# Kernel tuning notes

Measured on AMD Instinct MI355X. Metric: run time of the kernel, lower is better.

Reference implementation:

```python
import jax, jax.numpy as jnp
import numpy as np

BATCH, SEQ, D_IN, D_OUT = 32, 1024, 128, 128
NEG_SLOPE = 0.1


def setup_inputs() -> dict:
    key = jax.random.key(0)
    k1, k2, k3, k4 = jax.random.split(key, 4)
    nodes = jax.random.normal(k1, (BATCH, SEQ, D_IN), dtype=jnp.float32)
    adjacent = jax.random.randint(k2, (BATCH, SEQ, SEQ), 0, 2, dtype=jnp.int32)
    W = jax.random.normal(k3, (D_IN, D_OUT), dtype=jnp.float32) / np.sqrt(D_IN)
    B = jax.random.normal(k4, (D_IN, D_OUT), dtype=jnp.float32) / np.sqrt(D_IN)
    return {"nodes": nodes, "adjacent": adjacent, "W": W, "B": B}


def reference(nodes, adjacent, W, B):
    # mask[b, out, in] = 1 if edge (out -> in) present
    mask = (adjacent != 0).astype(nodes.dtype)
    # counts[b, in] = in-degree (number of 'out' neighbors pooled per target node)
    counts = mask.sum(axis=1)                               # [b, s_in]
    # segment-sum of neighbor features: pooled[b, in, d] = sum_out mask * nodes[b, out, d]
    pooled = jnp.einsum('boi,bod->bid', mask, nodes)        # [b, s_in, d]
    # mean over neighbors; nodes with zero degree get no pooled contribution
    pooled = jnp.where(counts[..., None] > 0,
                       pooled / jnp.maximum(counts, 1.0)[..., None],
                       jnp.zeros((), dtype=nodes.dtype))
    updated = nodes @ B + pooled @ W                        # [b, s, d_out]
    return jax.nn.leaky_relu(updated, negative_slope=NEG_SLOPE)
```

## Files before the change

### kernel.cpp

```cpp
#include <hip/hip_runtime.h>
#include <hip/hip_bf16.h>

#define SEQ 1024
#define DIM 128
#define NEG_SLOPE 0.1f

typedef __bf16 bf16x8 __attribute__((ext_vector_type(8)));
typedef float f32x4v __attribute__((ext_vector_type(4)));
typedef unsigned char uchar;

#define MASKQ_BYTES ((size_t)32 * 1024 * 1024)
#define NTQ_BYTES   ((size_t)32 * 128 * 1024)

__device__ __forceinline__ unsigned short bfb(float f) {
    __bf16 h = (__bf16)f;
    return __builtin_bit_cast(unsigned short, h);
}


__device__ __forceinline__ uchar f32_to_e4m3(float f) {
#if __has_builtin(__builtin_amdgcn_cvt_pk_fp8_f32)
    int r = __builtin_amdgcn_cvt_pk_fp8_f32(f, f, 0, false);
    return (uchar)(r & 0xff);
#else
    unsigned u = __builtin_bit_cast(unsigned, f);
    unsigned s = (u >> 24) & 0x80;
    int e = (u >> 23) & 0xff;
    unsigned m = u & 0x7fffff;
    int te = e - 120;
    if (te >= 1) {
        unsigned keep = m >> 20, rest = m & 0xfffff;
        keep += (rest > 0x80000u) || (rest == 0x80000u && (keep & 1));
        if (keep == 8) { keep = 0; ++te; }
        if (te > 15) return (uchar)(s | 0x7e);
        return (uchar)(s | (te << 3) | keep);
    }
    float af = f < 0 ? -f : f;
    int q = (int)(af * 512.0f + 0.5f);
    if (q > 7) q = 7;
    return (uchar)(s | q);
#endif
}

__global__ __launch_bounds__(256)
void transpose_adj(const int* __restrict__ adj, uchar* __restrict__ mq)
{
    __shared__ uchar lds[64][72];
    const int b  = blockIdx.x >> 8;
    const int ot = (blockIdx.x >> 4) & 15;
    const int it = blockIdx.x & 15;
    const int o0 = ot << 6, i0 = it << 6;
    const int t  = threadIdx.x;

    const int r0 = (t >> 4) << 2;
    const int c0 = (t & 15) << 2;
    const int* pa = adj + ((size_t)(b * SEQ + o0 + r0)) * SEQ + i0 + c0;
    int4 A[4];
    #pragma unroll
    for (int r = 0; r < 4; ++r) A[r] = *(const int4*)(pa + (size_t)r * SEQ);

    #pragma unroll
    for (int c = 0; c < 4; ++c) {
        unsigned w = 0;
        w |= (((const int*)&A[0])[c] != 0 ? 0x38u : 0u);
        w |= (((const int*)&A[1])[c] != 0 ? 0x38u : 0u) << 8;
        w |= (((const int*)&A[2])[c] != 0 ? 0x38u : 0u) << 16;
        w |= (((const int*)&A[3])[c] != 0 ? 0x38u : 0u) << 24;
        *(unsigned*)&lds[c0 + c][r0] = w;
    }
    __syncthreads();

    const int i_loc = t >> 2;
    const int quad  = t & 3;
    const uint2 lo = *(const uint2*)&lds[i_loc][quad * 8];
    const uint2 hi = *(const uint2*)&lds[i_loc][32 + quad * 8];
    uint4 outv; outv.x = lo.x; outv.y = lo.y; outv.z = hi.x; outv.w = hi.y;
    *(uint4*)(mq + ((size_t)(b * SEQ + i0 + i_loc)) * SEQ + o0 + quad * 16) = outv;
}

__global__ __launch_bounds__(256)
void transpose_nodes(const float* __restrict__ nodes, uchar* __restrict__ nq)
{
    __shared__ float lds[64][33];
    const int b  = blockIdx.x >> 6;
    const int ot = (blockIdx.x >> 2) & 15;
    const int dt = blockIdx.x & 3;
    const int o0 = ot << 6, d0 = dt << 5;
    const int t  = threadIdx.x;

    const float* src = nodes + ((size_t)(b * SEQ + o0)) * DIM + d0;
    #pragma unroll
    for (int p = 0; p < 8; ++p) {
        const int o = (t >> 5) + p * 8;
        const int d = t & 31;
        lds[o][d] = src[(size_t)o * DIM + d];
    }
    __syncthreads();

    const int d_loc = t >> 3;
    const int p0    = (t & 7) * 8;
    const int quad  = (t & 7) >> 1;
    const int half  = t & 1;
    const int ob    = half * 32 + quad * 8;
    union { uchar b[8]; uint2 u; } pk;
    #pragma unroll
    for (int j = 0; j < 8; ++j) pk.b[j] = f32_to_e4m3(lds[ob + j][d_loc]);
    *(uint2*)(nq + ((size_t)(b * DIM + d0 + d_loc)) * SEQ + o0 + p0) = pk.u;
}

__global__ __launch_bounds__(256)
void transpose_wb(const float* __restrict__ W, const float* __restrict__ Bm,
                  unsigned short* __restrict__ wt, unsigned short* __restrict__ bt)
{
    const int which = blockIdx.x & 1;
    const int slice = blockIdx.x >> 1;
    const float* in = which ? Bm : W;
    unsigned short* out = which ? bt : wt;
    const int base = slice * 1024;
    #pragma unroll
    for (int r = 0; r < 4; ++r) {
        const int idx = base + r * 256 + threadIdx.x;
        const int d = idx >> 7, k = idx & 127;
        out[idx] = bfb(in[k * DIM + d]);
    }
}

__device__ __forceinline__ long mk64(unsigned lo, unsigned hi) {
    return (long)(((unsigned long long)hi << 32) | lo);
}

__global__ __launch_bounds__(256, 2)
void gcn_main(const float* __restrict__ nodes,
              const uchar* __restrict__ mq,
              const uchar* __restrict__ nq,
              const unsigned short* __restrict__ wt,
              const unsigned short* __restrict__ bt,
              float* __restrict__ out)
{
    __shared__ unsigned short pooled[64][136];

    const int bid   = blockIdx.x;
    const int xcd   = bid & 7;
    const int slot  = bid >> 3;
    const int batch = ((slot >> 4) << 3) | xcd;
    const int mtile = slot & 15;
    const int i0    = mtile << 6;

    const int tid  = threadIdx.x;
    const int wave = tid >> 6;
    const int lane = tid & 63;
    const int wm   = wave >> 1;
    const int wn   = wave & 1;
    const int lrow = lane & 15;
    const int quad = lane >> 4;

    const uchar* __restrict__ mq_b = mq + (size_t)batch * SEQ * SEQ;
    const uchar* __restrict__ nq_b = nq + (size_t)batch * DIM * SEQ;
    const float* __restrict__ nodes_b = nodes + (size_t)batch * SEQ * DIM;

    f32x4v acc[2][4] = {};
    f32x4v acc_cnt[2] = {};
    const long ones = 0x3838383838383838L;

    const uchar* pa0 = mq_b + (size_t)(i0 + wm * 32 + lrow) * SEQ + quad * 16;
    const uchar* pb0 = nq_b + (size_t)(wn * 64 + lrow) * SEQ + quad * 16;

    #pragma unroll 4
    for (int n = 0; n < 16; ++n) {
        const int off = n * 64;
        uint4 a4[2], b4[4];
        #pragma unroll
        for (int mf = 0; mf < 2; ++mf)
            a4[mf] = *(const uint4*)(pa0 + (size_t)mf * 16 * SEQ + off);
        #pragma unroll
        for (int nf = 0; nf < 4; ++nf)
            b4[nf] = *(const uint4*)(pb0 + (size_t)nf * 16 * SEQ + off);
        #pragma unroll
        for (int half = 0; half < 2; ++half) {
            long a64[2], b64[4];
            #pragma unroll
            for (int mf = 0; mf < 2; ++mf)
                a64[mf] = half ? mk64(a4[mf].z, a4[mf].w) : mk64(a4[mf].x, a4[mf].y);
            #pragma unroll
            for (int nf = 0; nf < 4; ++nf)
                b64[nf] = half ? mk64(b4[nf].z, b4[nf].w) : mk64(b4[nf].x, b4[nf].y);
            #pragma unroll
            for (int mf = 0; mf < 2; ++mf) {
                #pragma unroll
                for (int nf = 0; nf < 4; ++nf)
                    acc[mf][nf] = __builtin_amdgcn_mfma_f32_16x16x32_fp8_fp8(
                        a64[mf], b64[nf], acc[mf][nf], 0, 0, 0);
                acc_cnt[mf] = __builtin_amdgcn_mfma_f32_16x16x32_fp8_fp8(
                    a64[mf], ones, acc_cnt[mf], 0, 0, 0);
            }
        }
    }

    #pragma unroll
    for (int mf = 0; mf < 2; ++mf) {
        #pragma unroll
        for (int r = 0; r < 4; ++r) {
            const int row = wm * 32 + mf * 16 + quad * 4 + r;
            const float cnt = acc_cnt[mf][r];
            const float inv = (cnt > 0.5f) ? 1.0f / cnt : 0.0f;
            #pragma unroll
            for (int nf = 0; nf < 4; ++nf) {
                const int col = wn * 64 + nf * 16 + lrow;
                pooled[row][col] = bfb(acc[mf][nf][r] * inv);
            }
        }
    }
    __syncthreads();

    f32x4v acc2[2][4] = {};
    const int d_b0 = wn * 64 + lrow;

    #pragma unroll
    for (int ks = 0; ks < 4; ++ks) {
        const int k0 = ks * 32 + quad * 8;
        bf16x8 av[2], av2[2], bw[4], bb[4];
        #pragma unroll
        for (int mf = 0; mf < 2; ++mf) {
            av[mf] = *(const bf16x8*)&pooled[wm * 32 + mf * 16 + lrow][k0];
            const float* p = nodes_b + (size_t)(i0 + wm * 32 + mf * 16 + lrow) * DIM + k0;
            const float4 f1 = *(const float4*)p;
            const float4 f2 = *(const float4*)(p + 4);
            av2[mf][0] = (__bf16)f1.x; av2[mf][1] = (__bf16)f1.y;
            av2[mf][2] = (__bf16)f1.z; av2[mf][3] = (__bf16)f1.w;
            av2[mf][4] = (__bf16)f2.x; av2[mf][5] = (__bf16)f2.y;
            av2[mf][6] = (__bf16)f2.z; av2[mf][7] = (__bf16)f2.w;
        }
        #pragma unroll
        for (int nf = 0; nf < 4; ++nf) {
            bw[nf] = *(const bf16x8*)(wt + (size_t)(d_b0 + nf * 16) * DIM + k0);
            bb[nf] = *(const bf16x8*)(bt + (size_t)(d_b0 + nf * 16) * DIM + k0);
        }
        #pragma unroll
        for (int mf = 0; mf < 2; ++mf)
            #pragma unroll
            for (int nf = 0; nf < 4; ++nf) {
                acc2[mf][nf] = __builtin_amdgcn_mfma_f32_16x16x32_bf16(av[mf],  bw[nf], acc2[mf][nf], 0, 0, 0);
                acc2[mf][nf] = __builtin_amdgcn_mfma_f32_16x16x32_bf16(av2[mf], bb[nf], acc2[mf][nf], 0, 0, 0);
            }
    }

    float* out_b = out + (size_t)batch * SEQ * DIM;
    #pragma unroll
    for (int mf = 0; mf < 2; ++mf) {
        #pragma unroll
        for (int nf = 0; nf < 4; ++nf) {
            const int col = wn * 64 + nf * 16 + lrow;
            #pragma unroll
            for (int r = 0; r < 4; ++r) {
                const int row = i0 + wm * 32 + mf * 16 + quad * 4 + r;
                const float x = acc2[mf][nf][r];
                out_b[(size_t)row * DIM + col] = (x > 0.0f) ? x : NEG_SLOPE * x;
            }
        }
    }
}

extern "C" void kernel_launch(void* const* d_in, const int* in_sizes, int n_in,
                              void* d_out, int out_size, void* d_ws, size_t ws_size,
                              hipStream_t stream) {
    const float* nodes = (const float*)d_in[0];
    const int*   adj   = (const int*)d_in[1];
    const float* W     = (const float*)d_in[2];
    const float* Bm    = (const float*)d_in[3];
    float*       out   = (float*)d_out;

    uchar* mq = (uchar*)d_ws;
    uchar* nq = mq + MASKQ_BYTES;
    unsigned short* wt = (unsigned short*)(nq + NTQ_BYTES);
    unsigned short* bt = wt + 16384;

    transpose_adj  <<<dim3(8192), dim3(256), 0, stream>>>(adj, mq);
    transpose_nodes<<<dim3(2048), dim3(256), 0, stream>>>(nodes, nq);
    transpose_wb   <<<dim3(32),   dim3(256), 0, stream>>>(W, Bm, wt, bt);
    gcn_main       <<<dim3(512),  dim3(256), 0, stream>>>(nodes, mq, nq, wt, bt, out);
}
```

Baseline: 255.2 us.

## Fuse adjacency mask transpose into main GCN kernel with LDS double buffer

Removes the separate adjacency-to-fp8 transpose kernel and its 32 MB intermediate buffer. The main kernel now reads int32 adjacency directly, builds the fp8 mask tile in LDS with double buffering, and prefetches the next chunk. The row tile shrinks to 32 with higher occupancy and twice as many blocks, and the node transpose permutation is simplified to match. This trades extra intermediate traffic for narrower global reads of adjacency and more repeated reads of the node operand.

```diff
diff --git a/kernel.cpp b/kernel.cpp
--- a/kernel.cpp
+++ b/kernel.cpp
@@ -9,14 +9,12 @@
 typedef float f32x4v __attribute__((ext_vector_type(4)));
 typedef unsigned char uchar;
 
-#define MASKQ_BYTES ((size_t)32 * 1024 * 1024)
-#define NTQ_BYTES   ((size_t)32 * 128 * 1024)
+#define NTQ_BYTES ((size_t)32 * 128 * 1024)
 
 __device__ __forceinline__ unsigned short bfb(float f) {
     __bf16 h = (__bf16)f;
     return __builtin_bit_cast(unsigned short, h);
 }
-
 
 __device__ __forceinline__ uchar f32_to_e4m3(float f) {
 #if __has_builtin(__builtin_amdgcn_cvt_pk_fp8_f32)
@@ -42,40 +40,8 @@
 #endif
 }
 
-__global__ __launch_bounds__(256)
-void transpose_adj(const int* __restrict__ adj, uchar* __restrict__ mq)
-{
-    __shared__ uchar lds[64][72];
-    const int b  = blockIdx.x >> 8;
-    const int ot = (blockIdx.x >> 4) & 15;
-    const int it = blockIdx.x & 15;
-    const int o0 = ot << 6, i0 = it << 6;
-    const int t  = threadIdx.x;
-
-    const int r0 = (t >> 4) << 2;
-    const int c0 = (t & 15) << 2;
-    const int* pa = adj + ((size_t)(b * SEQ + o0 + r0)) * SEQ + i0 + c0;
-    int4 A[4];
-    #pragma unroll
-    for (int r = 0; r < 4; ++r) A[r] = *(const int4*)(pa + (size_t)r * SEQ);
-
-    #pragma unroll
-    for (int c = 0; c < 4; ++c) {
-        unsigned w = 0;
-        w |= (((const int*)&A[0])[c] != 0 ? 0x38u : 0u);
-        w |= (((const int*)&A[1])[c] != 0 ? 0x38u : 0u) << 8;
-        w |= (((const int*)&A[2])[c] != 0 ? 0x38u : 0u) << 16;
-        w |= (((const int*)&A[3])[c] != 0 ? 0x38u : 0u) << 24;
-        *(unsigned*)&lds[c0 + c][r0] = w;
-    }
-    __syncthreads();
-
-    const int i_loc = t >> 2;
-    const int quad  = t & 3;
-    const uint2 lo = *(const uint2*)&lds[i_loc][quad * 8];
-    const uint2 hi = *(const uint2*)&lds[i_loc][32 + quad * 8];
-    uint4 outv; outv.x = lo.x; outv.y = lo.y; outv.z = hi.x; outv.w = hi.y;
-    *(uint4*)(mq + ((size_t)(b * SEQ + i0 + i_loc)) * SEQ + o0 + quad * 16) = outv;
+__device__ __forceinline__ long mk64(unsigned lo, unsigned hi) {
+    return (long)(((unsigned long long)hi << 32) | lo);
 }
 
 __global__ __launch_bounds__(256)
@@ -99,12 +65,9 @@
 
     const int d_loc = t >> 3;
     const int p0    = (t & 7) * 8;
-    const int quad  = (t & 7) >> 1;
-    const int half  = t & 1;
-    const int ob    = half * 32 + quad * 8;
     union { uchar b[8]; uint2 u; } pk;
     #pragma unroll
-    for (int j = 0; j < 8; ++j) pk.b[j] = f32_to_e4m3(lds[ob + j][d_loc]);
+    for (int j = 0; j < 8; ++j) pk.b[j] = f32_to_e4m3(lds[p0 + j][d_loc]);
     *(uint2*)(nq + ((size_t)(b * DIM + d0 + d_loc)) * SEQ + o0 + p0) = pk.u;
 }
 
@@ -125,110 +88,122 @@
     }
 }
 
-__device__ __forceinline__ long mk64(unsigned lo, unsigned hi) {
-    return (long)(((unsigned long long)hi << 32) | lo);
-}
-
-__global__ __launch_bounds__(256, 2)
+__global__ __launch_bounds__(256, 4)
 void gcn_main(const float* __restrict__ nodes,
-              const uchar* __restrict__ mq,
+              const int* __restrict__ adj,
               const uchar* __restrict__ nq,
               const unsigned short* __restrict__ wt,
               const unsigned short* __restrict__ bt,
               float* __restrict__ out)
 {
-    __shared__ unsigned short pooled[64][136];
+    __shared__ __align__(16) uchar mask_t[2][32][80];
+    __shared__ unsigned short pooled[32][136];
 
     const int bid   = blockIdx.x;
     const int xcd   = bid & 7;
     const int slot  = bid >> 3;
-    const int batch = ((slot >> 4) << 3) | xcd;
-    const int mtile = slot & 15;
-    const int i0    = mtile << 6;
+    const int batch = ((slot >> 5) << 3) | xcd;
+    const int itile = slot & 31;
+    const int i0    = itile << 5;
 
     const int tid  = threadIdx.x;
     const int wave = tid >> 6;
     const int lane = tid & 63;
-    const int wm   = wave >> 1;
+    const int wh   = wave >> 1;
     const int wn   = wave & 1;
     const int lrow = lane & 15;
     const int quad = lane >> 4;
 
-    const uchar* __restrict__ mq_b = mq + (size_t)batch * SEQ * SEQ;
-    const uchar* __restrict__ nq_b = nq + (size_t)batch * DIM * SEQ;
+    const int*   __restrict__ adj_b   = adj   + (size_t)batch * SEQ * SEQ;
+    const uchar* __restrict__ nq_b    = nq    + (size_t)batch * DIM * SEQ;
     const float* __restrict__ nodes_b = nodes + (size_t)batch * SEQ * DIM;
 
-    f32x4v acc[2][4] = {};
-    f32x4v acc_cnt[2] = {};
+    const int ig = tid & 15;
+    const int og = tid >> 4;
+
+    f32x4v acc[4] = {};
+    f32x4v acc_cnt = {};
     const long ones = 0x3838383838383838L;
 
-    const uchar* pa0 = mq_b + (size_t)(i0 + wm * 32 + lrow) * SEQ + quad * 16;
+    int2 A[4];
+    auto load_adj = [&](int oc) {
+        const int* pa = adj_b + (size_t)(oc + og * 4) * SEQ + i0 + ig * 2;
+        #pragma unroll
+        for (int rr = 0; rr < 4; ++rr) A[rr] = *(const int2*)(pa + (size_t)rr * SEQ);
+    };
+    uint4 Bv[4];
     const uchar* pb0 = nq_b + (size_t)(wn * 64 + lrow) * SEQ + quad * 16;
-
-    #pragma unroll 4
+    auto load_B = [&](int off) {
+        #pragma unroll
+        for (int nf = 0; nf < 4; ++nf)
+            Bv[nf] = *(const uint4*)(pb0 + (size_t)nf * 16 * SEQ + off);
+    };
+
+    load_adj(0);
+    load_B(0);
+
     for (int n = 0; n < 16; ++n) {
-        const int off = n * 64;
-        uint4 a4[2], b4[4];
-        #pragma unroll
-        for (int mf = 0; mf < 2; ++mf)
-            a4[mf] = *(const uint4*)(pa0 + (size_t)mf * 16 * SEQ + off);
-        #pragma unroll
-        for (int nf = 0; nf < 4; ++nf)
-            b4[nf] = *(const uint4*)(pb0 + (size_t)nf * 16 * SEQ + off);
+        const int buf = n & 1;
+        unsigned w0 = 0, w1 = 0;
+        #pragma unroll
+        for (int rr = 0; rr < 4; ++rr) {
+            w0 |= (A[rr].x != 0 ? 0x38u : 0u) << (8 * rr);
+            w1 |= (A[rr].y != 0 ? 0x38u : 0u) << (8 * rr);
+        }
+        *(unsigned*)&mask_t[buf][ig * 2][og * 4]     = w0;
+        *(unsigned*)&mask_t[buf][ig * 2 + 1][og * 4] = w1;
+        __syncthreads();
+
+        uint4 Bc[4];
+        #pragma unroll
+        for (int nf = 0; nf < 4; ++nf) Bc[nf] = Bv[nf];
+        if (n < 15) {
+            load_adj((n + 1) * 64);
+            load_B((n + 1) * 64);
+        }
+
+        const uint4 a4 = *(const uint4*)&mask_t[buf][wh * 16 + lrow][quad * 16];
         #pragma unroll
         for (int half = 0; half < 2; ++half) {
-            long a64[2], b64[4];
-            #pragma unroll
-            for (int mf = 0; mf < 2; ++mf)
-                a64[mf] = half ? mk64(a4[mf].z, a4[mf].w) : mk64(a4[mf].x, a4[mf].y);
-            #pragma unroll
-            for (int nf = 0; nf < 4; ++nf)
-                b64[nf] = half ? mk64(b4[nf].z, b4[nf].w) : mk64(b4[nf].x, b4[nf].y);
-            #pragma unroll
-            for (int mf = 0; mf < 2; ++mf) {
-                #pragma unroll
-                for (int nf = 0; nf < 4; ++nf)
-                    acc[mf][nf] = __builtin_amdgcn_mfma_f32_16x16x32_fp8_fp8(
-                        a64[mf], b64[nf], acc[mf][nf], 0, 0, 0);
-                acc_cnt[mf] = __builtin_amdgcn_mfma_f32_16x16x32_fp8_fp8(
-                    a64[mf], ones, acc_cnt[mf], 0, 0, 0);
-            }
-        }
-    }
-
-    #pragma unroll
-    for (int mf = 0; mf < 2; ++mf) {
-        #pragma unroll
-        for (int r = 0; r < 4; ++r) {
-            const int row = wm * 32 + mf * 16 + quad * 4 + r;
-            const float cnt = acc_cnt[mf][r];
-            const float inv = (cnt > 0.5f) ? 1.0f / cnt : 0.0f;
+            const long a64 = half ? mk64(a4.z, a4.w) : mk64(a4.x, a4.y);
             #pragma unroll
             for (int nf = 0; nf < 4; ++nf) {
-                const int col = wn * 64 + nf * 16 + lrow;
-                pooled[row][col] = bfb(acc[mf][nf][r] * inv);
+                const long b64 = half ? mk64(Bc[nf].z, Bc[nf].w) : mk64(Bc[nf].x, Bc[nf].y);
+                acc[nf] = __builtin_amdgcn_mfma_f32_16x16x32_fp8_fp8(a64, b64, acc[nf], 0, 0, 0);
             }
+            acc_cnt = __builtin_amdgcn_mfma_f32_16x16x32_fp8_fp8(a64, ones, acc_cnt, 0, 0, 0);
+        }
+    }
+
+    #pragma unroll
+    for (int r = 0; r < 4; ++r) {
+        const int row = wh * 16 + quad * 4 + r;
+        const float cnt = acc_cnt[r];
+        const float inv = (cnt > 0.5f) ? 1.0f / cnt : 0.0f;
+        #pragma unroll
+        for (int nf = 0; nf < 4; ++nf) {
+            const int col = wn * 64 + nf * 16 + lrow;
+            pooled[row][col] = bfb(acc[nf][r] * inv);
         }
     }
     __syncthreads();
 
-    f32x4v acc2[2][4] = {};
+    f32x4v acc2[4] = {};
     const int d_b0 = wn * 64 + lrow;
 
     #pragma unroll
     for (int ks = 0; ks < 4; ++ks) {
         const int k0 = ks * 32 + quad * 8;
-        bf16x8 av[2], av2[2], bw[4], bb[4];
-        #pragma unroll
-        for (int mf = 0; mf < 2; ++mf) {
-            av[mf] = *(const bf16x8*)&pooled[wm * 32 + mf * 16 + lrow][k0];
-            const float* p = nodes_b + (size_t)(i0 + wm * 32 + mf * 16 + lrow) * DIM + k0;
+        bf16x8 av, av2, bw[4], bb[4];
+        av = *(const bf16x8*)&pooled[wh * 16 + lrow][k0];
+        {
+            const float* p = nodes_b + (size_t)(i0 + wh * 16 + lrow) * DIM + k0;
             const float4 f1 = *(const float4*)p;
             const float4 f2 = *(const float4*)(p + 4);
-            av2[mf][0] = (__bf16)f1.x; av2[mf][1] = (__bf16)f1.y;
-            av2[mf][2] = (__bf16)f1.z; av2[mf][3] = (__bf16)f1.w;
-            av2[mf][4] = (__bf16)f2.x; av2[mf][5] = (__bf16)f2.y;
-            av2[mf][6] = (__bf16)f2.z; av2[mf][7] = (__bf16)f2.w;
+            av2[0] = (__bf16)f1.x; av2[1] = (__bf16)f1.y;
+            av2[2] = (__bf16)f1.z; av2[3] = (__bf16)f1.w;
+            av2[4] = (__bf16)f2.x; av2[5] = (__bf16)f2.y;
+            av2[6] = (__bf16)f2.z; av2[7] = (__bf16)f2.w;
         }
         #pragma unroll
         for (int nf = 0; nf < 4; ++nf) {
@@ -236,26 +211,21 @@
             bb[nf] = *(const bf16x8*)(bt + (size_t)(d_b0 + nf * 16) * DIM + k0);
         }
         #pragma unroll
-        for (int mf = 0; mf < 2; ++mf)
-            #pragma unroll
-            for (int nf = 0; nf < 4; ++nf) {
-                acc2[mf][nf] = __builtin_amdgcn_mfma_f32_16x16x32_bf16(av[mf],  bw[nf], acc2[mf][nf], 0, 0, 0);
-                acc2[mf][nf] = __builtin_amdgcn_mfma_f32_16x16x32_bf16(av2[mf], bb[nf], acc2[mf][nf], 0, 0, 0);
-            }
+        for (int nf = 0; nf < 4; ++nf) {
+            acc2[nf] = __builtin_amdgcn_mfma_f32_16x16x32_bf16(av,  bw[nf], acc2[nf], 0, 0, 0);
+            acc2[nf] = __builtin_amdgcn_mfma_f32_16x16x32_bf16(av2, bb[nf], acc2[nf], 0, 0, 0);
+        }
     }
 
     float* out_b = out + (size_t)batch * SEQ * DIM;
     #pragma unroll
-    for (int mf = 0; mf < 2; ++mf) {
-        #pragma unroll
-        for (int nf = 0; nf < 4; ++nf) {
-            const int col = wn * 64 + nf * 16 + lrow;
-            #pragma unroll
-            for (int r = 0; r < 4; ++r) {
-                const int row = i0 + wm * 32 + mf * 16 + quad * 4 + r;
-                const float x = acc2[mf][nf][r];
-                out_b[(size_t)row * DIM + col] = (x > 0.0f) ? x : NEG_SLOPE * x;
-            }
+    for (int nf = 0; nf < 4; ++nf) {
+        const int col = wn * 64 + nf * 16 + lrow;
+        #pragma unroll
+        for (int r = 0; r < 4; ++r) {
+            const int row = i0 + wh * 16 + quad * 4 + r;
+            const float x = acc2[nf][r];
+            out_b[(size_t)row * DIM + col] = (x > 0.0f) ? x : NEG_SLOPE * x;
         }
     }
 }
@@ -269,13 +239,11 @@
     const float* Bm    = (const float*)d_in[3];
     float*       out   = (float*)d_out;
 
-    uchar* mq = (uchar*)d_ws;
-    uchar* nq = mq + MASKQ_BYTES;
+    uchar* nq = (uchar*)d_ws;
     unsigned short* wt = (unsigned short*)(nq + NTQ_BYTES);
     unsigned short* bt = wt + 16384;
 
-    transpose_adj  <<<dim3(8192), dim3(256), 0, stream>>>(adj, mq);
     transpose_nodes<<<dim3(2048), dim3(256), 0, stream>>>(nodes, nq);
     transpose_wb   <<<dim3(32),   dim3(256), 0, stream>>>(W, Bm, wt, bt);
-    gcn_main       <<<dim3(512),  dim3(256), 0, stream>>>(nodes, mq, nq, wt, bt, out);
-}
+    gcn_main       <<<dim3(1024), dim3(256), 0, stream>>>(nodes, adj, nq, wt, bt, out);
+}
```

Result: faster. 248.3 us (-2.7%).
